# Kernel tuning notes

Measured on AMD Instinct MI355X. Metric: run time of the kernel, lower is better.

## Reference

```python
import jax, jax.numpy as jnp
import numpy as np

B, S, D = 1, 2048, 1024   # batch, seq_len, d_model
E, F, TOP_K = 8, 4096, 2  # num_experts, d_ff, top_k


def setup_inputs() -> dict:
    key = jax.random.key(0)
    k0, k1, k2, k3, k4 = jax.random.split(key, 5)
    s = 0.02
    x = jax.random.normal(k0, (B, S, D), jnp.float32)
    Wr = jax.random.normal(k1, (D, E), jnp.float32) * s          # router
    W1 = jax.random.normal(k2, (E, D, F), jnp.float32) * s       # gate proj per expert
    W3 = jax.random.normal(k3, (E, D, F), jnp.float32) * s       # up proj per expert
    W2 = jax.random.normal(k4, (E, F, D), jnp.float32) * s       # down proj per expert
    return {"x": x, "Wr": Wr, "W1": W1, "W2": W2, "W3": W3}


def reference(x, Wr, W1, W2, W3):
    b, s, d = x.shape
    e = Wr.shape[1]
    xt = x.reshape(b * s, d)                       # [T, D]
    logits = xt @ Wr                               # [T, E]
    top_v, top_i = jax.lax.top_k(logits, TOP_K)    # [T, K]
    probs = jax.nn.softmax(top_v, axis=-1)         # softmax over selected experts
    # combine[t, e] = prob of expert e for token t (0 if not selected)
    combine = jnp.sum(probs[..., None] * jax.nn.one_hot(top_i, e, dtype=xt.dtype), axis=1)  # [T, E]
    # SwiGLU FFN per expert (dense grouped-GEMM form of the gather/scatter loop)
    h = jnp.einsum('td,edf->etf', xt, W1)          # [E, T, F]
    g = jnp.einsum('td,edf->etf', xt, W3)          # [E, T, F]
    y = jnp.einsum('etf,efd->etd', jax.nn.silu(h) * g, W2)  # [E, T, D]
    out = jnp.einsum('etd,te->td', y, combine)     # weighted combine
    return out.reshape(b, s, d)
```

## Files before the change

### kernel.cpp

```cpp
#include <hip/hip_runtime.h>
#include <hip/hip_bf16.h>

#define T_TOK 2048
#define DDIM  1024
#define NEXP  8
#define FDIM  4096
#define ROWS  (4096 + 256)

typedef __attribute__((ext_vector_type(8))) short bf16x8;
typedef __attribute__((ext_vector_type(4))) float f32x4;

#define SBW(n) ((((n) >> 3) ^ (n)) & 7)

__device__ __forceinline__ unsigned short f2b(float f) {
  union { float f; unsigned u; } v; v.f = f;
  unsigned r = v.u + 0x7FFF + ((v.u >> 16) & 1);
  return (unsigned short)(r >> 16);
}
__device__ __forceinline__ float b2f(unsigned short s) {
  union { unsigned u; float f; } v; v.u = ((unsigned)s) << 16;
  return v.f;
}
__device__ __forceinline__ unsigned cvtpk(float lo, float hi) {
  unsigned r;
  asm("v_cvt_pk_bf16_f32 %0, %1, %2" : "=v"(r) : "v"(lo), "v"(hi));
  return r;
}
__device__ __forceinline__ void gl16(const unsigned short* g, unsigned short* l) {
  __builtin_amdgcn_global_load_lds(
      (const __attribute__((address_space(1))) unsigned int*)(const void*)g,
      (__attribute__((address_space(3))) unsigned int*)(void*)l, 16, 0, 0);
}
__device__ __forceinline__ bf16x8 pack8(const float4* br, int c) {
  union { bf16x8 v; unsigned u[4]; } p;
  p.u[0] = cvtpk((&br[0].x)[c], (&br[1].x)[c]);
  p.u[1] = cvtpk((&br[2].x)[c], (&br[3].x)[c]);
  p.u[2] = cvtpk((&br[4].x)[c], (&br[5].x)[c]);
  p.u[3] = cvtpk((&br[6].x)[c], (&br[7].x)[c]);
  return p.v;
}

__global__ void router_kernel(const float* __restrict__ x, const float* __restrict__ Wr,
                              int* __restrict__ cnt, int* __restrict__ tok,
                              float* __restrict__ prb) {
  int t = (blockIdx.x * blockDim.x + threadIdx.x) >> 6;
  int lane = threadIdx.x & 63;
  if (t >= T_TOK) return;
  const float* xr = x + (size_t)t * DDIM;
  float acc[NEXP];
#pragma unroll
  for (int e = 0; e < NEXP; ++e) acc[e] = 0.f;
#pragma unroll
  for (int i = 0; i < 4; ++i) {
    int d0 = lane * 16 + i * 4;
    float4 xv = *reinterpret_cast<const float4*>(xr + d0);
#pragma unroll
    for (int j = 0; j < 4; ++j) {
      float xd = (&xv.x)[j];
      float4 w0 = *reinterpret_cast<const float4*>(Wr + (size_t)(d0 + j) * NEXP);
      float4 w1 = *reinterpret_cast<const float4*>(Wr + (size_t)(d0 + j) * NEXP + 4);
      acc[0] += xd * w0.x; acc[1] += xd * w0.y; acc[2] += xd * w0.z; acc[3] += xd * w0.w;
      acc[4] += xd * w1.x; acc[5] += xd * w1.y; acc[6] += xd * w1.z; acc[7] += xd * w1.w;
    }
  }
#pragma unroll
  for (int off = 32; off >= 1; off >>= 1)
#pragma unroll
    for (int e = 0; e < NEXP; ++e) acc[e] += __shfl_down(acc[e], off);
  if (lane == 0) {
    float v0 = -1e30f, v1 = -1e30f; int i0 = 0, i1 = 0;
#pragma unroll
    for (int e = 0; e < NEXP; ++e) {
      float v = acc[e];
      if (v > v0)      { v1 = v0; i1 = i0; v0 = v; i0 = e; }
      else if (v > v1) { v1 = v; i1 = e; }
    }
    float e1 = __expf(v1 - v0);
    float p0 = 1.f / (1.f + e1);
    float p1 = e1 * p0;
    int s0 = atomicAdd(&cnt[i0], 1);
    tok[i0 * T_TOK + s0] = t; prb[i0 * T_TOK + s0] = p0;
    int s1 = atomicAdd(&cnt[i1], 1);
    tok[i1 * T_TOK + s1] = t; prb[i1 * T_TOK + s1] = p1;
  }
}

__global__ void gather_x_kernel(const float* __restrict__ x, const int* __restrict__ cnt,
                                const int* __restrict__ tok, unsigned short* __restrict__ xg) {
  int gs = blockIdx.x * 4 + (threadIdx.x >> 6);
  int lane = threadIdx.x & 63;
  int s = gs, e = 0;
#pragma unroll
  for (int i = 0; i < NEXP - 1; ++i) {
    int c = cnt[i];
    bool go = (e == i) && (s >= c);
    if (go) { s -= c; e = i + 1; }
  }
  int tk = tok[e * T_TOK + s];
  const float* src = x + (size_t)tk * DDIM;
  unsigned short* dst = xg + (size_t)gs * DDIM;
#pragma unroll
  for (int it = 0; it < 4; ++it) {
    float4 v = *reinterpret_cast<const float4*>(src + it * 256 + lane * 4);
    uint2 p;
    p.x = cvtpk(v.x, v.y);
    p.y = cvtpk(v.z, v.w);
    *reinterpret_cast<uint2*>(dst + it * 256 + lane * 4) = p;
  }
}

__global__ __launch_bounds__(256, 3)
void gemm1ab_kernel(const unsigned short* __restrict__ xg,
                    const float* __restrict__ W1, const float* __restrict__ W3,
                    const int* __restrict__ cnt,
                    unsigned short* __restrict__ act) {
  const int e = blockIdx.z;
  const int cn = cnt[e];
  const int r0 = blockIdx.y * 128;
  if (r0 >= cn) return;
  const int n0 = blockIdx.x * 64;
  int off = 0;
#pragma unroll
  for (int i = 0; i < NEXP; ++i) off += (i < e) ? cnt[i] : 0;

  __shared__ __align__(16) unsigned short sA[128 * 64];
  __shared__ __align__(16) unsigned short sB1[64 * 64];
  __shared__ __align__(16) unsigned short sB3[64 * 64];

  const int tid = threadIdx.x;
  const int lane = tid & 63;
  const int wid = tid >> 6;
  const int wm = wid >> 1, wn = wid & 1;

  const unsigned short* asrc[4];
#pragma unroll
  for (int i = 0; i < 4; ++i) {
    int row = (4 * wid + i) * 8 + (lane >> 3);
    int sl = (lane & 7) ^ (row & 7);
    asrc[i] = xg + (size_t)(off + r0 + row) * DDIM + sl * 8;
  }

  const int lt = tid & 127;
  const int ko = lt >> 4;
  const int nc = (lt & 15) * 4;
  const float* bp = ((tid < 128) ? W1 : W3) + ((size_t)e * DDIM + 8 * ko) * FDIM + n0 + nc;
  unsigned short* wb = (tid < 128) ? sB1 : sB3;
  int woff[4];
#pragma unroll
  for (int c = 0; c < 4; ++c) woff[c] = (nc + c) * 64 + ((ko ^ SBW(nc + c)) * 8);

  float4 br[8];
#define LOADB1(K0)                                                              \
  _Pragma("unroll") for (int r = 0; r < 8; ++r)                                 \
      br[r] = *reinterpret_cast<const float4*>(bp + (size_t)((K0) + r) * FDIM);
#define WRITEB1()                                                               \
  _Pragma("unroll") for (int c = 0; c < 4; ++c)                                 \
      *reinterpret_cast<bf16x8*>(wb + woff[c]) = pack8(br, c);
#define STAGEA1(K0)                                                             \
  _Pragma("unroll") for (int i = 0; i < 4; ++i)                                 \
      gl16(asrc[i] + (K0), &sA[(4 * wid + i) * 512]);

  f32x4 ah[4][2], ag[4][2];
#pragma unroll
  for (int m = 0; m < 4; ++m)
#pragma unroll
    for (int n = 0; n < 2; ++n) { ah[m][n] = (f32x4){0,0,0,0}; ag[m][n] = (f32x4){0,0,0,0}; }

  LOADB1(0);

  for (int k0 = 0; k0 < DDIM; k0 += 64) {
    WRITEB1();
    STAGEA1(k0);
    __syncthreads();
    if (k0 + 64 < DDIM) LOADB1(k0 + 64);
#pragma unroll
    for (int kk = 0; kk < 2; ++kk) {
      int kc8 = kk * 4 + (lane >> 4);
      bf16x8 a[4], b1[2], b3[2];
#pragma unroll
      for (int m = 0; m < 4; ++m) {
        int row = wm * 64 + m * 16 + (lane & 15);
        a[m] = *reinterpret_cast<const bf16x8*>(&sA[row * 64 + ((kc8 ^ (row & 7)) * 8)]);
      }
#pragma unroll
      for (int n = 0; n < 2; ++n) {
        int rowb = wn * 32 + n * 16 + (lane & 15);
        int offb = rowb * 64 + ((kc8 ^ SBW(rowb)) * 8);
        b1[n] = *reinterpret_cast<const bf16x8*>(&sB1[offb]);
        b3[n] = *reinterpret_cast<const bf16x8*>(&sB3[offb]);
      }
#pragma unroll
      for (int m = 0; m < 4; ++m)
#pragma unroll
        for (int n = 0; n < 2; ++n) {
          ah[m][n] = __builtin_amdgcn_mfma_f32_16x16x32_bf16(a[m], b1[n], ah[m][n], 0, 0, 0);
          ag[m][n] = __builtin_amdgcn_mfma_f32_16x16x32_bf16(a[m], b3[n], ag[m][n], 0, 0, 0);
        }
    }
    __syncthreads();
  }
#pragma unroll
  for (int m = 0; m < 4; ++m)
#pragma unroll
    for (int j = 0; j < 4; ++j) {
      int rloc = wm * 64 + m * 16 + (lane >> 4) * 4 + j;
      int s = r0 + rloc;
      if (s < cn) {
        unsigned short* orow = act + (size_t)(off + s) * FDIM + n0 + wn * 32 + (lane & 15);
#pragma unroll
        for (int n = 0; n < 2; ++n) {
          float hv = ah[m][n][j];
          float gv = ag[m][n][j];
          float sg = hv / (1.f + __expf(-hv));
          orow[n * 16] = f2b(sg * gv);
        }
      }
    }
}

__global__ __launch_bounds__(256, 3)
void gemm2d_kernel(const unsigned short* __restrict__ act, const float* __restrict__ W2,
                   const int* __restrict__ cnt, const int* __restrict__ tok,
                   const float* __restrict__ prb, float* __restrict__ out) {
  const int e = blockIdx.z >> 1;
  const int sp = blockIdx.z & 1;
  const int cn = cnt[e];
  const int r0 = blockIdx.y * 128;
  if (r0 >= cn) return;
  const int n0 = blockIdx.x * 128;
  const int kbase = sp * (FDIM / 2);
  int off = 0;
#pragma unroll
  for (int i = 0; i < NEXP; ++i) off += (i < e) ? cnt[i] : 0;

  __shared__ __align__(16) unsigned short sA[128 * 64];
  __shared__ __align__(16) unsigned short sB[128 * 64];

  const int tid = threadIdx.x;
  const int lane = tid & 63;
  const int wid = tid >> 6;
  const int wm = wid >> 1, wn = wid & 1;

  const unsigned short* asrc[4];
#pragma unroll
  for (int i = 0; i < 4; ++i) {
    int row = (4 * wid + i) * 8 + (lane >> 3);
    int sl = (lane & 7) ^ (row & 7);
    asrc[i] = act + (size_t)(off + r0 + row) * FDIM + kbase + sl * 8;
  }

  const int ko = tid >> 5;
  const int nc = (tid & 31) * 4;
  const float* bp = W2 + ((size_t)e * FDIM + kbase + 8 * ko) * DDIM + n0 + nc;
  int woff[4];
#pragma unroll
  for (int c = 0; c < 4; ++c) woff[c] = (nc + c) * 64 + ((ko ^ SBW(nc + c)) * 8);

  float4 br[8];
#define LOADB2(K0)                                                              \
  _Pragma("unroll") for (int r = 0; r < 8; ++r)                                 \
      br[r] = *reinterpret_cast<const float4*>(bp + (size_t)((K0) + r) * DDIM);
#define WRITEB2()                                                               \
  _Pragma("unroll") for (int c = 0; c < 4; ++c)                                 \
      *reinterpret_cast<bf16x8*>(&sB[woff[c]]) = pack8(br, c);
#define STAGEA2(K0)                                                             \
  _Pragma("unroll") for (int i = 0; i < 4; ++i)                                 \
      gl16(asrc[i] + (K0), &sA[(4 * wid + i) * 512]);

  f32x4 acc[4][4];
#pragma unroll
  for (int m = 0; m < 4; ++m)
#pragma unroll
    for (int n = 0; n < 4; ++n) acc[m][n] = (f32x4){0,0,0,0};

  LOADB2(0);

  for (int k0 = 0; k0 < FDIM / 2; k0 += 64) {
    WRITEB2();
    STAGEA2(k0);
    __syncthreads();
    if (k0 + 64 < FDIM / 2) LOADB2(k0 + 64);
#pragma unroll
    for (int kk = 0; kk < 2; ++kk) {
      int kc8 = kk * 4 + (lane >> 4);
      bf16x8 a[4], b[4];
#pragma unroll
      for (int m = 0; m < 4; ++m) {
        int row = wm * 64 + m * 16 + (lane & 15);
        a[m] = *reinterpret_cast<const bf16x8*>(&sA[row * 64 + ((kc8 ^ (row & 7)) * 8)]);
      }
#pragma unroll
      for (int n = 0; n < 4; ++n) {
        int col = wn * 64 + n * 16 + (lane & 15);
        b[n] = *reinterpret_cast<const bf16x8*>(&sB[col * 64 + ((kc8 ^ SBW(col)) * 8)]);
      }
#pragma unroll
      for (int m = 0; m < 4; ++m)
#pragma unroll
        for (int n = 0; n < 4; ++n)
          acc[m][n] = __builtin_amdgcn_mfma_f32_16x16x32_bf16(a[m], b[n], acc[m][n], 0, 0, 0);
    }
    __syncthreads();
  }
#pragma unroll
  for (int m = 0; m < 4; ++m)
#pragma unroll
    for (int j = 0; j < 4; ++j) {
      int rloc = wm * 64 + m * 16 + (lane >> 4) * 4 + j;
      int s = r0 + rloc;
      if (s < cn) {
        int tkn = tok[e * T_TOK + s];
        float p = prb[e * T_TOK + s];
        float* orow = out + (size_t)tkn * DDIM + n0 + wn * 64 + (lane & 15);
#pragma unroll
        for (int n = 0; n < 4; ++n) atomicAdd(&orow[n * 16], p * acc[m][n][j]);
      }
    }
}

extern "C" void kernel_launch(void* const* d_in, const int* in_sizes, int n_in,
                              void* d_out, int out_size, void* d_ws, size_t ws_size,
                              hipStream_t stream) {
  const float* x  = (const float*)d_in[0];
  const float* Wr = (const float*)d_in[1];
  const float* W1 = (const float*)d_in[2];
  const float* W2 = (const float*)d_in[3];
  const float* W3 = (const float*)d_in[4];
  float* out = (float*)d_out;

  char* ws = (char*)d_ws;
  int*   cnt = (int*)ws;
  int*   tok = (int*)(ws + 1024);
  float* prb = (float*)(ws + 1024 + 65536);
  unsigned short* xg  = (unsigned short*)(ws + 256 * 1024);
  unsigned short* act = xg + (size_t)ROWS * DDIM;

  hipMemsetAsync(cnt, 0, NEXP * sizeof(int), stream);
  hipMemsetAsync(d_out, 0, (size_t)out_size * sizeof(float), stream);

  router_kernel<<<T_TOK / 4, 256, 0, stream>>>(x, Wr, cnt, tok, prb);
  gather_x_kernel<<<(2 * T_TOK) / 4, 256, 0, stream>>>(x, cnt, tok, xg);
  gemm1ab_kernel<<<dim3(FDIM / 64, 16, NEXP), 256, 0, stream>>>(xg, W1, W3, cnt, act);
  gemm2d_kernel<<<dim3(DDIM / 128, 16, NEXP * 2), 256, 0, stream>>>(act, W2, cnt, tok, prb, out);
}
```

Baseline: 294.7 us.

## Double-buffer A tile and prefetch B two stages ahead in expert GEMMs

```diff
diff --git a/kernel.cpp b/kernel.cpp
--- a/kernel.cpp
+++ b/kernel.cpp
@@ -39,6 +39,16 @@
   p.u[3] = cvtpk((&br[6].x)[c], (&br[7].x)[c]);
   return p.v;
 }
+
+#define BAR_KEEP12()                                              \
+  __builtin_amdgcn_sched_barrier(0);                              \
+  asm volatile("s_waitcnt vmcnt(12) lgkmcnt(0)" ::: "memory");    \
+  __builtin_amdgcn_s_barrier();                                   \
+  __builtin_amdgcn_sched_barrier(0)
+#define BAR_PLAIN()                                               \
+  __builtin_amdgcn_sched_barrier(0);                              \
+  __builtin_amdgcn_s_barrier();                                   \
+  __builtin_amdgcn_sched_barrier(0)
 
 __global__ void router_kernel(const float* __restrict__ x, const float* __restrict__ Wr,
                               int* __restrict__ cnt, int* __restrict__ tok,
@@ -123,7 +133,7 @@
 #pragma unroll
   for (int i = 0; i < NEXP; ++i) off += (i < e) ? cnt[i] : 0;
 
-  __shared__ __align__(16) unsigned short sA[128 * 64];
+  __shared__ __align__(16) unsigned short sA[2][128 * 64];
   __shared__ __align__(16) unsigned short sB1[64 * 64];
   __shared__ __align__(16) unsigned short sB3[64 * 64];
 
@@ -149,16 +159,16 @@
 #pragma unroll
   for (int c = 0; c < 4; ++c) woff[c] = (nc + c) * 64 + ((ko ^ SBW(nc + c)) * 8);
 
-  float4 br[8];
-#define LOADB1(K0)                                                              \
+  float4 brA[8], brB[8];
+#define LOADB1(BR, K0)                                                          \
   _Pragma("unroll") for (int r = 0; r < 8; ++r)                                 \
-      br[r] = *reinterpret_cast<const float4*>(bp + (size_t)((K0) + r) * FDIM);
-#define WRITEB1()                                                               \
+      BR[r] = *reinterpret_cast<const float4*>(bp + (size_t)((K0) + r) * FDIM);
+#define WRITEB1(BR)                                                             \
   _Pragma("unroll") for (int c = 0; c < 4; ++c)                                 \
-      *reinterpret_cast<bf16x8*>(wb + woff[c]) = pack8(br, c);
-#define STAGEA1(K0)                                                             \
+      *reinterpret_cast<bf16x8*>(wb + woff[c]) = pack8(BR, c);
+#define STAGEA1(K0, BUF)                                                        \
   _Pragma("unroll") for (int i = 0; i < 4; ++i)                                 \
-      gl16(asrc[i] + (K0), &sA[(4 * wid + i) * 512]);
+      gl16(asrc[i] + (K0), &sA[BUF][(4 * wid + i) * 512]);
 
   f32x4 ah[4][2], ag[4][2];
 #pragma unroll
@@ -166,39 +176,51 @@
 #pragma unroll
     for (int n = 0; n < 2; ++n) { ah[m][n] = (f32x4){0,0,0,0}; ag[m][n] = (f32x4){0,0,0,0}; }
 
-  LOADB1(0);
-
-  for (int k0 = 0; k0 < DDIM; k0 += 64) {
-    WRITEB1();
-    STAGEA1(k0);
-    __syncthreads();
-    if (k0 + 64 < DDIM) LOADB1(k0 + 64);
-#pragma unroll
-    for (int kk = 0; kk < 2; ++kk) {
-      int kc8 = kk * 4 + (lane >> 4);
-      bf16x8 a[4], b1[2], b3[2];
-#pragma unroll
-      for (int m = 0; m < 4; ++m) {
-        int row = wm * 64 + m * 16 + (lane & 15);
-        a[m] = *reinterpret_cast<const bf16x8*>(&sA[row * 64 + ((kc8 ^ (row & 7)) * 8)]);
-      }
-#pragma unroll
-      for (int n = 0; n < 2; ++n) {
-        int rowb = wn * 32 + n * 16 + (lane & 15);
-        int offb = rowb * 64 + ((kc8 ^ SBW(rowb)) * 8);
-        b1[n] = *reinterpret_cast<const bf16x8*>(&sB1[offb]);
-        b3[n] = *reinterpret_cast<const bf16x8*>(&sB3[offb]);
-      }
-#pragma unroll
-      for (int m = 0; m < 4; ++m)
-#pragma unroll
-        for (int n = 0; n < 2; ++n) {
-          ah[m][n] = __builtin_amdgcn_mfma_f32_16x16x32_bf16(a[m], b1[n], ah[m][n], 0, 0, 0);
-          ag[m][n] = __builtin_amdgcn_mfma_f32_16x16x32_bf16(a[m], b3[n], ag[m][n], 0, 0, 0);
-        }
-    }
-    __syncthreads();
-  }
+#define MFMA1(CUR)                                                              \
+  _Pragma("unroll") for (int kk = 0; kk < 2; ++kk) {                            \
+    int kc8 = kk * 4 + (lane >> 4);                                             \
+    bf16x8 a[4], b1[2], b3[2];                                                  \
+    _Pragma("unroll") for (int m = 0; m < 4; ++m) {                             \
+      int row = wm * 64 + m * 16 + (lane & 15);                                 \
+      a[m] = *reinterpret_cast<const bf16x8*>(&sA[CUR][row * 64 + ((kc8 ^ (row & 7)) * 8)]); \
+    }                                                                           \
+    _Pragma("unroll") for (int n = 0; n < 2; ++n) {                             \
+      int rowb = wn * 32 + n * 16 + (lane & 15);                                \
+      int offb = rowb * 64 + ((kc8 ^ SBW(rowb)) * 8);                           \
+      b1[n] = *reinterpret_cast<const bf16x8*>(&sB1[offb]);                     \
+      b3[n] = *reinterpret_cast<const bf16x8*>(&sB3[offb]);                     \
+    }                                                                           \
+    _Pragma("unroll") for (int m = 0; m < 4; ++m)                               \
+      _Pragma("unroll") for (int n = 0; n < 2; ++n) {                           \
+        ah[m][n] = __builtin_amdgcn_mfma_f32_16x16x32_bf16(a[m], b1[n], ah[m][n], 0, 0, 0); \
+        ag[m][n] = __builtin_amdgcn_mfma_f32_16x16x32_bf16(a[m], b3[n], ag[m][n], 0, 0, 0); \
+      }                                                                         \
+  }
+
+#define HALF1(K0, BR, CUR)                                                      \
+  WRITEB1(BR);                               \
+  STAGEA1(((K0) + 64) & (DDIM - 1), (CUR) ^ 1);       \
+  LOADB1(BR, ((K0) + 128) & (DDIM - 1));              \
+  BAR_KEEP12();                                                                 \
+  __builtin_amdgcn_s_setprio(1);                                                \
+  MFMA1(CUR);                                                                   \
+  __builtin_amdgcn_s_setprio(0);                                                \
+  BAR_PLAIN();
+
+  LOADB1(brA, 0);
+  LOADB1(brB, 64);
+  STAGEA1(0, 0);
+
+  for (int k0 = 0; k0 < DDIM; k0 += 128) {
+    HALF1(k0, brA, 0);
+    HALF1(k0 + 64, brB, 1);
+  }
+#undef HALF1
+#undef MFMA1
+#undef LOADB1
+#undef WRITEB1
+#undef STAGEA1
+
 #pragma unroll
   for (int m = 0; m < 4; ++m)
 #pragma unroll
@@ -233,7 +255,7 @@
 #pragma unroll
   for (int i = 0; i < NEXP; ++i) off += (i < e) ? cnt[i] : 0;
 
-  __shared__ __align__(16) unsigned short sA[128 * 64];
+  __shared__ __align__(16) unsigned short sA[2][128 * 64];
   __shared__ __align__(16) unsigned short sB[128 * 64];
 
   const int tid = threadIdx.x;
@@ -256,16 +278,16 @@
 #pragma unroll
   for (int c = 0; c < 4; ++c) woff[c] = (nc + c) * 64 + ((ko ^ SBW(nc + c)) * 8);
 
-  float4 br[8];
-#define LOADB2(K0)                                                              \
+  float4 brA[8], brB[8];
+#define LOADB2(BR, K0)                                                          \
   _Pragma("unroll") for (int r = 0; r < 8; ++r)                                 \
-      br[r] = *reinterpret_cast<const float4*>(bp + (size_t)((K0) + r) * DDIM);
-#define WRITEB2()                                                               \
+      BR[r] = *reinterpret_cast<const float4*>(bp + (size_t)((K0) + r) * DDIM);
+#define WRITEB2(BR)                                                             \
   _Pragma("unroll") for (int c = 0; c < 4; ++c)                                 \
-      *reinterpret_cast<bf16x8*>(&sB[woff[c]]) = pack8(br, c);
-#define STAGEA2(K0)                                                             \
+      *reinterpret_cast<bf16x8*>(&sB[woff[c]]) = pack8(BR, c);
+#define STAGEA2(K0, BUF)                                                        \
   _Pragma("unroll") for (int i = 0; i < 4; ++i)                                 \
-      gl16(asrc[i] + (K0), &sA[(4 * wid + i) * 512]);
+      gl16(asrc[i] + (K0), &sA[BUF][(4 * wid + i) * 512]);
 
   f32x4 acc[4][4];
 #pragma unroll
@@ -273,35 +295,47 @@
 #pragma unroll
     for (int n = 0; n < 4; ++n) acc[m][n] = (f32x4){0,0,0,0};
 
-  LOADB2(0);
-
-  for (int k0 = 0; k0 < FDIM / 2; k0 += 64) {
-    WRITEB2();
-    STAGEA2(k0);
-    __syncthreads();
-    if (k0 + 64 < FDIM / 2) LOADB2(k0 + 64);
-#pragma unroll
-    for (int kk = 0; kk < 2; ++kk) {
-      int kc8 = kk * 4 + (lane >> 4);
-      bf16x8 a[4], b[4];
-#pragma unroll
-      for (int m = 0; m < 4; ++m) {
-        int row = wm * 64 + m * 16 + (lane & 15);
-        a[m] = *reinterpret_cast<const bf16x8*>(&sA[row * 64 + ((kc8 ^ (row & 7)) * 8)]);
-      }
-#pragma unroll
-      for (int n = 0; n < 4; ++n) {
-        int col = wn * 64 + n * 16 + (lane & 15);
-        b[n] = *reinterpret_cast<const bf16x8*>(&sB[col * 64 + ((kc8 ^ SBW(col)) * 8)]);
-      }
-#pragma unroll
-      for (int m = 0; m < 4; ++m)
-#pragma unroll
-        for (int n = 0; n < 4; ++n)
-          acc[m][n] = __builtin_amdgcn_mfma_f32_16x16x32_bf16(a[m], b[n], acc[m][n], 0, 0, 0);
-    }
-    __syncthreads();
-  }
+#define MFMA2(CUR)                                                              \
+  _Pragma("unroll") for (int kk = 0; kk < 2; ++kk) {                            \
+    int kc8 = kk * 4 + (lane >> 4);                                             \
+    bf16x8 a[4], b[4];                                                          \
+    _Pragma("unroll") for (int m = 0; m < 4; ++m) {                             \
+      int row = wm * 64 + m * 16 + (lane & 15);                                 \
+      a[m] = *reinterpret_cast<const bf16x8*>(&sA[CUR][row * 64 + ((kc8 ^ (row & 7)) * 8)]); \
+    }                                                                           \
+    _Pragma("unroll") for (int n = 0; n < 4; ++n) {                             \
+      int col = wn * 64 + n * 16 + (lane & 15);                                 \
+      b[n] = *reinterpret_cast<const bf16x8*>(&sB[col * 64 + ((kc8 ^ SBW(col)) * 8)]); \
+    }                                                                           \
+    _Pragma("unroll") for (int m = 0; m < 4; ++m)                               \
+      _Pragma("unroll") for (int n = 0; n < 4; ++n)                             \
+        acc[m][n] = __builtin_amdgcn_mfma_f32_16x16x32_bf16(a[m], b[n], acc[m][n], 0, 0, 0); \
+  }
+
+#define HALF2(K0, BR, CUR)                                                      \
+  WRITEB2(BR);                                                                  \
+  STAGEA2(((K0) + 64) & (FDIM / 2 - 1), (CUR) ^ 1);                             \
+  LOADB2(BR, ((K0) + 128) & (FDIM / 2 - 1));                                    \
+  BAR_KEEP12();                                                                 \
+  __builtin_amdgcn_s_setprio(1);                                                \
+  MFMA2(CUR);                                                                   \
+  __builtin_amdgcn_s_setprio(0);                                                \
+  BAR_PLAIN();
+
+  LOADB2(brA, 0);
+  LOADB2(brB, 64);
+  STAGEA2(0, 0);
+
+  for (int k0 = 0; k0 < FDIM / 2; k0 += 128) {
+    HALF2(k0, brA, 0);
+    HALF2(k0 + 64, brB, 1);
+  }
+#undef HALF2
+#undef MFMA2
+#undef LOADB2
+#undef WRITEB2
+#undef STAGEA2
+
 #pragma unroll
   for (int m = 0; m < 4; ++m)
 #pragma unroll
```

Result: slower. 672.5 us (+128.2%).

## Use 512-thread blocks with 256-row tiles and split warp roles for loading

Applied to the files above, without the earlier changes.

```diff
diff --git a/kernel.cpp b/kernel.cpp
--- a/kernel.cpp
+++ b/kernel.cpp
@@ -109,45 +109,47 @@
   }
 }
 
-__global__ __launch_bounds__(256, 3)
+__global__ __launch_bounds__(512, 2)
 void gemm1ab_kernel(const unsigned short* __restrict__ xg,
                     const float* __restrict__ W1, const float* __restrict__ W3,
                     const int* __restrict__ cnt,
                     unsigned short* __restrict__ act) {
   const int e = blockIdx.z;
   const int cn = cnt[e];
-  const int r0 = blockIdx.y * 128;
+  const int r0 = blockIdx.y * 256;
   if (r0 >= cn) return;
   const int n0 = blockIdx.x * 64;
   int off = 0;
 #pragma unroll
   for (int i = 0; i < NEXP; ++i) off += (i < e) ? cnt[i] : 0;
 
-  __shared__ __align__(16) unsigned short sA[128 * 64];
+  __shared__ __align__(16) unsigned short sA[256 * 64];
   __shared__ __align__(16) unsigned short sB1[64 * 64];
   __shared__ __align__(16) unsigned short sB3[64 * 64];
 
   const int tid = threadIdx.x;
   const int lane = tid & 63;
-  const int wid = tid >> 6;
-  const int wm = wid >> 1, wn = wid & 1;
-
-  const unsigned short* asrc[4];
-#pragma unroll
-  for (int i = 0; i < 4; ++i) {
-    int row = (4 * wid + i) * 8 + (lane >> 3);
-    int sl = (lane & 7) ^ (row & 7);
-    asrc[i] = xg + (size_t)(off + r0 + row) * DDIM + sl * 8;
-  }
+  const int w = tid >> 6;
 
   const int lt = tid & 127;
   const int ko = lt >> 4;
   const int nc = (lt & 15) * 4;
-  const float* bp = ((tid < 128) ? W1 : W3) + ((size_t)e * DDIM + 8 * ko) * FDIM + n0 + nc;
-  unsigned short* wb = (tid < 128) ? sB1 : sB3;
+  const float* bp = ((tid & 128) ? W3 : W1) + ((size_t)e * DDIM + 8 * ko) * FDIM + n0 + nc;
+  unsigned short* wb = (tid & 128) ? sB3 : sB1;
   int woff[4];
 #pragma unroll
   for (int c = 0; c < 4; ++c) woff[c] = (nc + c) * 64 + ((ko ^ SBW(nc + c)) * 8);
+
+  const unsigned short* asrc[8];
+  {
+    int w4 = (tid >> 6) & 3;
+#pragma unroll
+    for (int i = 0; i < 8; ++i) {
+      int row = (w4 * 8 + i) * 8 + (lane >> 3);
+      int sl = (lane & 7) ^ (row & 7);
+      asrc[i] = xg + (size_t)(off + r0 + row) * DDIM + sl * 8;
+    }
+  }
 
   float4 br[8];
 #define LOADB1(K0)                                                              \
@@ -157,58 +159,61 @@
   _Pragma("unroll") for (int c = 0; c < 4; ++c)                                 \
       *reinterpret_cast<bf16x8*>(wb + woff[c]) = pack8(br, c);
 #define STAGEA1(K0)                                                             \
-  _Pragma("unroll") for (int i = 0; i < 4; ++i)                                 \
-      gl16(asrc[i] + (K0), &sA[(4 * wid + i) * 512]);
-
-  f32x4 ah[4][2], ag[4][2];
-#pragma unroll
-  for (int m = 0; m < 4; ++m)
-#pragma unroll
-    for (int n = 0; n < 2; ++n) { ah[m][n] = (f32x4){0,0,0,0}; ag[m][n] = (f32x4){0,0,0,0}; }
-
-  LOADB1(0);
+  {                                                                             \
+    int w4s = (tid >> 6) & 3;                                                   \
+    _Pragma("unroll") for (int i = 0; i < 8; ++i)                               \
+        gl16(asrc[i] + (K0), &sA[(w4s * 8 + i) * 512]);                         \
+  }
+
+  f32x4 ah[2][4], ag[2][4];
+#pragma unroll
+  for (int m = 0; m < 2; ++m)
+#pragma unroll
+    for (int n = 0; n < 4; ++n) { ah[m][n] = (f32x4){0,0,0,0}; ag[m][n] = (f32x4){0,0,0,0}; }
+
+  if (w < 4) LOADB1(0);
 
   for (int k0 = 0; k0 < DDIM; k0 += 64) {
-    WRITEB1();
-    STAGEA1(k0);
+    if (w < 4) { WRITEB1(); } else { STAGEA1(k0); }
     __syncthreads();
-    if (k0 + 64 < DDIM) LOADB1(k0 + 64);
+    if (w < 4 && k0 + 64 < DDIM) LOADB1(k0 + 64);
 #pragma unroll
     for (int kk = 0; kk < 2; ++kk) {
       int kc8 = kk * 4 + (lane >> 4);
-      bf16x8 a[4], b1[2], b3[2];
-#pragma unroll
-      for (int m = 0; m < 4; ++m) {
-        int row = wm * 64 + m * 16 + (lane & 15);
+      bf16x8 a[2], b1[4], b3[4];
+#pragma unroll
+      for (int m = 0; m < 2; ++m) {
+        int row = w * 32 + m * 16 + (lane & 15);
         a[m] = *reinterpret_cast<const bf16x8*>(&sA[row * 64 + ((kc8 ^ (row & 7)) * 8)]);
       }
 #pragma unroll
-      for (int n = 0; n < 2; ++n) {
-        int rowb = wn * 32 + n * 16 + (lane & 15);
+      for (int n = 0; n < 4; ++n) {
+        int rowb = n * 16 + (lane & 15);
         int offb = rowb * 64 + ((kc8 ^ SBW(rowb)) * 8);
         b1[n] = *reinterpret_cast<const bf16x8*>(&sB1[offb]);
         b3[n] = *reinterpret_cast<const bf16x8*>(&sB3[offb]);
       }
 #pragma unroll
-      for (int m = 0; m < 4; ++m)
-#pragma unroll
-        for (int n = 0; n < 2; ++n) {
+      for (int m = 0; m < 2; ++m)
+#pragma unroll
+        for (int n = 0; n < 4; ++n) {
           ah[m][n] = __builtin_amdgcn_mfma_f32_16x16x32_bf16(a[m], b1[n], ah[m][n], 0, 0, 0);
           ag[m][n] = __builtin_amdgcn_mfma_f32_16x16x32_bf16(a[m], b3[n], ag[m][n], 0, 0, 0);
         }
     }
     __syncthreads();
   }
-#pragma unroll
-  for (int m = 0; m < 4; ++m)
+
+#pragma unroll
+  for (int m = 0; m < 2; ++m)
 #pragma unroll
     for (int j = 0; j < 4; ++j) {
-      int rloc = wm * 64 + m * 16 + (lane >> 4) * 4 + j;
+      int rloc = w * 32 + m * 16 + (lane >> 4) * 4 + j;
       int s = r0 + rloc;
       if (s < cn) {
-        unsigned short* orow = act + (size_t)(off + s) * FDIM + n0 + wn * 32 + (lane & 15);
-#pragma unroll
-        for (int n = 0; n < 2; ++n) {
+        unsigned short* orow = act + (size_t)(off + s) * FDIM + n0 + (lane & 15);
+#pragma unroll
+        for (int n = 0; n < 4; ++n) {
           float hv = ah[m][n][j];
           float gv = ag[m][n][j];
           float sg = hv / (1.f + __expf(-hv));
@@ -218,43 +223,46 @@
     }
 }
 
-__global__ __launch_bounds__(256, 3)
+__global__ __launch_bounds__(512, 2)
 void gemm2d_kernel(const unsigned short* __restrict__ act, const float* __restrict__ W2,
                    const int* __restrict__ cnt, const int* __restrict__ tok,
                    const float* __restrict__ prb, float* __restrict__ out) {
-  const int e = blockIdx.z >> 1;
-  const int sp = blockIdx.z & 1;
+  const int e = blockIdx.z >> 2;
+  const int sp = blockIdx.z & 3;
   const int cn = cnt[e];
-  const int r0 = blockIdx.y * 128;
+  const int r0 = blockIdx.y * 256;
   if (r0 >= cn) return;
   const int n0 = blockIdx.x * 128;
-  const int kbase = sp * (FDIM / 2);
+  const int kbase = sp * (FDIM / 4);
   int off = 0;
 #pragma unroll
   for (int i = 0; i < NEXP; ++i) off += (i < e) ? cnt[i] : 0;
 
-  __shared__ __align__(16) unsigned short sA[128 * 64];
+  __shared__ __align__(16) unsigned short sA[256 * 64];
   __shared__ __align__(16) unsigned short sB[128 * 64];
 
   const int tid = threadIdx.x;
   const int lane = tid & 63;
-  const int wid = tid >> 6;
-  const int wm = wid >> 1, wn = wid & 1;
-
-  const unsigned short* asrc[4];
-#pragma unroll
-  for (int i = 0; i < 4; ++i) {
-    int row = (4 * wid + i) * 8 + (lane >> 3);
-    int sl = (lane & 7) ^ (row & 7);
-    asrc[i] = act + (size_t)(off + r0 + row) * FDIM + kbase + sl * 8;
-  }
-
-  const int ko = tid >> 5;
-  const int nc = (tid & 31) * 4;
+  const int w = tid >> 6;
+
+  const int lt = tid & 255;
+  const int ko = lt >> 5;
+  const int nc = (lt & 31) * 4;
   const float* bp = W2 + ((size_t)e * FDIM + kbase + 8 * ko) * DDIM + n0 + nc;
   int woff[4];
 #pragma unroll
   for (int c = 0; c < 4; ++c) woff[c] = (nc + c) * 64 + ((ko ^ SBW(nc + c)) * 8);
+
+  const unsigned short* asrc[8];
+  {
+    int w4 = (tid >> 6) & 3;
+#pragma unroll
+    for (int i = 0; i < 8; ++i) {
+      int row = (w4 * 8 + i) * 8 + (lane >> 3);
+      int sl = (lane & 7) ^ (row & 7);
+      asrc[i] = act + (size_t)(off + r0 + row) * FDIM + kbase + sl * 8;
+    }
+  }
 
   float4 br[8];
 #define LOADB2(K0)                                                              \
@@ -264,56 +272,59 @@
   _Pragma("unroll") for (int c = 0; c < 4; ++c)                                 \
       *reinterpret_cast<bf16x8*>(&sB[woff[c]]) = pack8(br, c);
 #define STAGEA2(K0)                                                             \
-  _Pragma("unroll") for (int i = 0; i < 4; ++i)                                 \
-      gl16(asrc[i] + (K0), &sA[(4 * wid + i) * 512]);
-
-  f32x4 acc[4][4];
-#pragma unroll
-  for (int m = 0; m < 4; ++m)
-#pragma unroll
-    for (int n = 0; n < 4; ++n) acc[m][n] = (f32x4){0,0,0,0};
-
-  LOADB2(0);
-
-  for (int k0 = 0; k0 < FDIM / 2; k0 += 64) {
-    WRITEB2();
-    STAGEA2(k0);
+  {                                                                             \
+    int w4s = (tid >> 6) & 3;                                                   \
+    _Pragma("unroll") for (int i = 0; i < 8; ++i)                               \
+        gl16(asrc[i] + (K0), &sA[(w4s * 8 + i) * 512]);                         \
+  }
+
+  f32x4 acc[2][8];
+#pragma unroll
+  for (int m = 0; m < 2; ++m)
+#pragma unroll
+    for (int n = 0; n < 8; ++n) acc[m][n] = (f32x4){0,0,0,0};
+
+  if (w < 4) LOADB2(0);
+
+  for (int k0 = 0; k0 < FDIM / 4; k0 += 64) {
+    if (w < 4) { WRITEB2(); } else { STAGEA2(k0); }
     __syncthreads();
-    if (k0 + 64 < FDIM / 2) LOADB2(k0 + 64);
+    if (w < 4 && k0 + 64 < FDIM / 4) LOADB2(k0 + 64);
 #pragma unroll
     for (int kk = 0; kk < 2; ++kk) {
       int kc8 = kk * 4 + (lane >> 4);
-      bf16x8 a[4], b[4];
-#pragma unroll
-      for (int m = 0; m < 4; ++m) {
-        int row = wm * 64 + m * 16 + (lane & 15);
+      bf16x8 a[2], b[8];
+#pragma unroll
+      for (int m = 0; m < 2; ++m) {
+        int row = w * 32 + m * 16 + (lane & 15);
         a[m] = *reinterpret_cast<const bf16x8*>(&sA[row * 64 + ((kc8 ^ (row & 7)) * 8)]);
       }
 #pragma unroll
-      for (int n = 0; n < 4; ++n) {
-        int col = wn * 64 + n * 16 + (lane & 15);
+      for (int n = 0; n < 8; ++n) {
+        int col = n * 16 + (lane & 15);
         b[n] = *reinterpret_cast<const bf16x8*>(&sB[col * 64 + ((kc8 ^ SBW(col)) * 8)]);
       }
 #pragma unroll
-      for (int m = 0; m < 4; ++m)
-#pragma unroll
-        for (int n = 0; n < 4; ++n)
+      for (int m = 0; m < 2; ++m)
+#pragma unroll
+        for (int n = 0; n < 8; ++n)
           acc[m][n] = __builtin_amdgcn_mfma_f32_16x16x32_bf16(a[m], b[n], acc[m][n], 0, 0, 0);
     }
     __syncthreads();
   }
-#pragma unroll
-  for (int m = 0; m < 4; ++m)
+
+#pragma unroll
+  for (int m = 0; m < 2; ++m)
 #pragma unroll
     for (int j = 0; j < 4; ++j) {
-      int rloc = wm * 64 + m * 16 + (lane >> 4) * 4 + j;
+      int rloc = w * 32 + m * 16 + (lane >> 4) * 4 + j;
       int s = r0 + rloc;
       if (s < cn) {
         int tkn = tok[e * T_TOK + s];
         float p = prb[e * T_TOK + s];
-        float* orow = out + (size_t)tkn * DDIM + n0 + wn * 64 + (lane & 15);
-#pragma unroll
-        for (int n = 0; n < 4; ++n) atomicAdd(&orow[n * 16], p * acc[m][n][j]);
+        float* orow = out + (size_t)tkn * DDIM + n0 + (lane & 15);
+#pragma unroll
+        for (int n = 0; n < 8; ++n) atomicAdd(&orow[n * 16], p * acc[m][n][j]);
       }
     }
 }
@@ -340,6 +351,6 @@
 
   router_kernel<<<T_TOK / 4, 256, 0, stream>>>(x, Wr, cnt, tok, prb);
   gather_x_kernel<<<(2 * T_TOK) / 4, 256, 0, stream>>>(x, cnt, tok, xg);
-  gemm1ab_kernel<<<dim3(FDIM / 64, 16, NEXP), 256, 0, stream>>>(xg, W1, W3, cnt, act);
-  gemm2d_kernel<<<dim3(DDIM / 128, 16, NEXP * 2), 256, 0, stream>>>(act, W2, cnt, tok, prb, out);
-}
+  gemm1ab_kernel<<<dim3(FDIM / 64, 8, NEXP), 512, 0, stream>>>(xg, W1, W3, cnt, act);
+  gemm2d_kernel<<<dim3(DDIM / 128, 8, NEXP * 4), 512, 0, stream>>>(act, W2, cnt, tok, prb, out);
+}
```

Result: slower. 348.8 us (+18.4%).

## Use 32x32x16 MFMA and 256-row M tiles in both expert GEMMs

Applied to the files above, without the earlier changes.

```diff
diff --git a/kernel.cpp b/kernel.cpp
--- a/kernel.cpp
+++ b/kernel.cpp
@@ -9,6 +9,7 @@
 
 typedef __attribute__((ext_vector_type(8))) short bf16x8;
 typedef __attribute__((ext_vector_type(4))) float f32x4;
+typedef __attribute__((ext_vector_type(16))) float f32x16;
 
 #define SBW(n) ((((n) >> 3) ^ (n)) & 7)
 
@@ -109,33 +110,32 @@
   }
 }
 
-__global__ __launch_bounds__(256, 3)
+__global__ __launch_bounds__(256, 2)
 void gemm1ab_kernel(const unsigned short* __restrict__ xg,
                     const float* __restrict__ W1, const float* __restrict__ W3,
                     const int* __restrict__ cnt,
                     unsigned short* __restrict__ act) {
   const int e = blockIdx.z;
   const int cn = cnt[e];
-  const int r0 = blockIdx.y * 128;
+  const int r0 = blockIdx.y * 256;
   if (r0 >= cn) return;
   const int n0 = blockIdx.x * 64;
   int off = 0;
 #pragma unroll
   for (int i = 0; i < NEXP; ++i) off += (i < e) ? cnt[i] : 0;
 
-  __shared__ __align__(16) unsigned short sA[128 * 64];
+  __shared__ __align__(16) unsigned short sA[256 * 64];
   __shared__ __align__(16) unsigned short sB1[64 * 64];
   __shared__ __align__(16) unsigned short sB3[64 * 64];
 
   const int tid = threadIdx.x;
   const int lane = tid & 63;
   const int wid = tid >> 6;
-  const int wm = wid >> 1, wn = wid & 1;
-
-  const unsigned short* asrc[4];
-#pragma unroll
-  for (int i = 0; i < 4; ++i) {
-    int row = (4 * wid + i) * 8 + (lane >> 3);
+
+  const unsigned short* asrc[8];
+#pragma unroll
+  for (int i = 0; i < 8; ++i) {
+    int row = (wid * 8 + i) * 8 + (lane >> 3);
     int sl = (lane & 7) ^ (row & 7);
     asrc[i] = xg + (size_t)(off + r0 + row) * DDIM + sl * 8;
   }
@@ -157,16 +157,22 @@
   _Pragma("unroll") for (int c = 0; c < 4; ++c)                                 \
       *reinterpret_cast<bf16x8*>(wb + woff[c]) = pack8(br, c);
 #define STAGEA1(K0)                                                             \
-  _Pragma("unroll") for (int i = 0; i < 4; ++i)                                 \
-      gl16(asrc[i] + (K0), &sA[(4 * wid + i) * 512]);
-
-  f32x4 ah[4][2], ag[4][2];
-#pragma unroll
-  for (int m = 0; m < 4; ++m)
-#pragma unroll
-    for (int n = 0; n < 2; ++n) { ah[m][n] = (f32x4){0,0,0,0}; ag[m][n] = (f32x4){0,0,0,0}; }
+  _Pragma("unroll") for (int i = 0; i < 8; ++i)                                 \
+      gl16(asrc[i] + (K0), &sA[(wid * 8 + i) * 512]);
+
+  f32x16 ah[2][2], ag[2][2];
+#pragma unroll
+  for (int m = 0; m < 2; ++m)
+#pragma unroll
+    for (int n = 0; n < 2; ++n) {
+      ah[m][n] = (f32x16)(0.f);
+      ag[m][n] = (f32x16)(0.f);
+    }
 
   LOADB1(0);
+
+  const int l31 = lane & 31;
+  const int khalf = lane >> 5;
 
   for (int k0 = 0; k0 < DDIM; k0 += 64) {
     WRITEB1();
@@ -174,58 +180,59 @@
     __syncthreads();
     if (k0 + 64 < DDIM) LOADB1(k0 + 64);
 #pragma unroll
-    for (int kk = 0; kk < 2; ++kk) {
-      int kc8 = kk * 4 + (lane >> 4);
-      bf16x8 a[4], b1[2], b3[2];
-#pragma unroll
-      for (int m = 0; m < 4; ++m) {
-        int row = wm * 64 + m * 16 + (lane & 15);
-        a[m] = *reinterpret_cast<const bf16x8*>(&sA[row * 64 + ((kc8 ^ (row & 7)) * 8)]);
+    for (int kk = 0; kk < 4; ++kk) {
+      int s = kk * 2 + khalf;
+      bf16x8 a[2], b1[2], b3[2];
+#pragma unroll
+      for (int m = 0; m < 2; ++m) {
+        int row = wid * 64 + m * 32 + l31;
+        a[m] = *reinterpret_cast<const bf16x8*>(&sA[row * 64 + ((s ^ (row & 7)) * 8)]);
       }
 #pragma unroll
       for (int n = 0; n < 2; ++n) {
-        int rowb = wn * 32 + n * 16 + (lane & 15);
-        int offb = rowb * 64 + ((kc8 ^ SBW(rowb)) * 8);
+        int rowb = n * 32 + l31;
+        int offb = rowb * 64 + ((s ^ SBW(rowb)) * 8);
         b1[n] = *reinterpret_cast<const bf16x8*>(&sB1[offb]);
         b3[n] = *reinterpret_cast<const bf16x8*>(&sB3[offb]);
       }
 #pragma unroll
-      for (int m = 0; m < 4; ++m)
+      for (int m = 0; m < 2; ++m)
 #pragma unroll
         for (int n = 0; n < 2; ++n) {
-          ah[m][n] = __builtin_amdgcn_mfma_f32_16x16x32_bf16(a[m], b1[n], ah[m][n], 0, 0, 0);
-          ag[m][n] = __builtin_amdgcn_mfma_f32_16x16x32_bf16(a[m], b3[n], ag[m][n], 0, 0, 0);
+          ah[m][n] = __builtin_amdgcn_mfma_f32_32x32x16_bf16(a[m], b1[n], ah[m][n], 0, 0, 0);
+          ag[m][n] = __builtin_amdgcn_mfma_f32_32x32x16_bf16(a[m], b3[n], ag[m][n], 0, 0, 0);
         }
     }
     __syncthreads();
   }
-#pragma unroll
-  for (int m = 0; m < 4; ++m)
-#pragma unroll
-    for (int j = 0; j < 4; ++j) {
-      int rloc = wm * 64 + m * 16 + (lane >> 4) * 4 + j;
+
+#pragma unroll
+  for (int m = 0; m < 2; ++m)
+#pragma unroll
+    for (int r = 0; r < 16; ++r) {
+      int rloc = wid * 64 + m * 32 + (r & 3) + 8 * (r >> 2) + 4 * khalf;
       int s = r0 + rloc;
       if (s < cn) {
-        unsigned short* orow = act + (size_t)(off + s) * FDIM + n0 + wn * 32 + (lane & 15);
+        unsigned short* orow = act + (size_t)(off + s) * FDIM + n0 + l31;
 #pragma unroll
         for (int n = 0; n < 2; ++n) {
-          float hv = ah[m][n][j];
-          float gv = ag[m][n][j];
+          float hv = ah[m][n][r];
+          float gv = ag[m][n][r];
           float sg = hv / (1.f + __expf(-hv));
-          orow[n * 16] = f2b(sg * gv);
+          orow[n * 32] = f2b(sg * gv);
         }
       }
     }
 }
 
-__global__ __launch_bounds__(256, 3)
+__global__ __launch_bounds__(256, 2)
 void gemm2d_kernel(const unsigned short* __restrict__ act, const float* __restrict__ W2,
                    const int* __restrict__ cnt, const int* __restrict__ tok,
                    const float* __restrict__ prb, float* __restrict__ out) {
   const int e = blockIdx.z >> 1;
   const int sp = blockIdx.z & 1;
   const int cn = cnt[e];
-  const int r0 = blockIdx.y * 128;
+  const int r0 = blockIdx.y * 256;
   if (r0 >= cn) return;
   const int n0 = blockIdx.x * 128;
   const int kbase = sp * (FDIM / 2);
@@ -233,18 +240,17 @@
 #pragma unroll
   for (int i = 0; i < NEXP; ++i) off += (i < e) ? cnt[i] : 0;
 
-  __shared__ __align__(16) unsigned short sA[128 * 64];
+  __shared__ __align__(16) unsigned short sA[256 * 64];
   __shared__ __align__(16) unsigned short sB[128 * 64];
 
   const int tid = threadIdx.x;
   const int lane = tid & 63;
   const int wid = tid >> 6;
-  const int wm = wid >> 1, wn = wid & 1;
-
-  const unsigned short* asrc[4];
-#pragma unroll
-  for (int i = 0; i < 4; ++i) {
-    int row = (4 * wid + i) * 8 + (lane >> 3);
+
+  const unsigned short* asrc[8];
+#pragma unroll
+  for (int i = 0; i < 8; ++i) {
+    int row = (wid * 8 + i) * 8 + (lane >> 3);
     int sl = (lane & 7) ^ (row & 7);
     asrc[i] = act + (size_t)(off + r0 + row) * FDIM + kbase + sl * 8;
   }
@@ -264,16 +270,19 @@
   _Pragma("unroll") for (int c = 0; c < 4; ++c)                                 \
       *reinterpret_cast<bf16x8*>(&sB[woff[c]]) = pack8(br, c);
 #define STAGEA2(K0)                                                             \
-  _Pragma("unroll") for (int i = 0; i < 4; ++i)                                 \
-      gl16(asrc[i] + (K0), &sA[(4 * wid + i) * 512]);
-
-  f32x4 acc[4][4];
-#pragma unroll
-  for (int m = 0; m < 4; ++m)
-#pragma unroll
-    for (int n = 0; n < 4; ++n) acc[m][n] = (f32x4){0,0,0,0};
+  _Pragma("unroll") for (int i = 0; i < 8; ++i)                                 \
+      gl16(asrc[i] + (K0), &sA[(wid * 8 + i) * 512]);
+
+  f32x16 acc[2][4];
+#pragma unroll
+  for (int m = 0; m < 2; ++m)
+#pragma unroll
+    for (int n = 0; n < 4; ++n) acc[m][n] = (f32x16)(0.f);
 
   LOADB2(0);
+
+  const int l31 = lane & 31;
+  const int khalf = lane >> 5;
 
   for (int k0 = 0; k0 < FDIM / 2; k0 += 64) {
     WRITEB2();
@@ -281,39 +290,40 @@
     __syncthreads();
     if (k0 + 64 < FDIM / 2) LOADB2(k0 + 64);
 #pragma unroll
-    for (int kk = 0; kk < 2; ++kk) {
-      int kc8 = kk * 4 + (lane >> 4);
-      bf16x8 a[4], b[4];
-#pragma unroll
-      for (int m = 0; m < 4; ++m) {
-        int row = wm * 64 + m * 16 + (lane & 15);
-        a[m] = *reinterpret_cast<const bf16x8*>(&sA[row * 64 + ((kc8 ^ (row & 7)) * 8)]);
+    for (int kk = 0; kk < 4; ++kk) {
+      int s = kk * 2 + khalf;
+      bf16x8 a[2], b[4];
+#pragma unroll
+      for (int m = 0; m < 2; ++m) {
+        int row = wid * 64 + m * 32 + l31;
+        a[m] = *reinterpret_cast<const bf16x8*>(&sA[row * 64 + ((s ^ (row & 7)) * 8)]);
       }
 #pragma unroll
       for (int n = 0; n < 4; ++n) {
-        int col = wn * 64 + n * 16 + (lane & 15);
-        b[n] = *reinterpret_cast<const bf16x8*>(&sB[col * 64 + ((kc8 ^ SBW(col)) * 8)]);
-      }
-#pragma unroll
-      for (int m = 0; m < 4; ++m)
+        int col = n * 32 + l31;
+        b[n] = *reinterpret_cast<const bf16x8*>(&sB[col * 64 + ((s ^ SBW(col)) * 8)]);
+      }
+#pragma unroll
+      for (int m = 0; m < 2; ++m)
 #pragma unroll
         for (int n = 0; n < 4; ++n)
-          acc[m][n] = __builtin_amdgcn_mfma_f32_16x16x32_bf16(a[m], b[n], acc[m][n], 0, 0, 0);
+          acc[m][n] = __builtin_amdgcn_mfma_f32_32x32x16_bf16(a[m], b[n], acc[m][n], 0, 0, 0);
     }
     __syncthreads();
   }
-#pragma unroll
-  for (int m = 0; m < 4; ++m)
-#pragma unroll
-    for (int j = 0; j < 4; ++j) {
-      int rloc = wm * 64 + m * 16 + (lane >> 4) * 4 + j;
+
+#pragma unroll
+  for (int m = 0; m < 2; ++m)
+#pragma unroll
+    for (int r = 0; r < 16; ++r) {
+      int rloc = wid * 64 + m * 32 + (r & 3) + 8 * (r >> 2) + 4 * khalf;
       int s = r0 + rloc;
       if (s < cn) {
         int tkn = tok[e * T_TOK + s];
         float p = prb[e * T_TOK + s];
-        float* orow = out + (size_t)tkn * DDIM + n0 + wn * 64 + (lane & 15);
-#pragma unroll
-        for (int n = 0; n < 4; ++n) atomicAdd(&orow[n * 16], p * acc[m][n][j]);
+        float* orow = out + (size_t)tkn * DDIM + n0 + l31;
+#pragma unroll
+        for (int n = 0; n < 4; ++n) atomicAdd(&orow[n * 32], p * acc[m][n][r]);
       }
     }
 }
@@ -340,6 +350,6 @@
 
   router_kernel<<<T_TOK / 4, 256, 0, stream>>>(x, Wr, cnt, tok, prb);
   gather_x_kernel<<<(2 * T_TOK) / 4, 256, 0, stream>>>(x, cnt, tok, xg);
-  gemm1ab_kernel<<<dim3(FDIM / 64, 16, NEXP), 256, 0, stream>>>(xg, W1, W3, cnt, act);
-  gemm2d_kernel<<<dim3(DDIM / 128, 16, NEXP * 2), 256, 0, stream>>>(act, W2, cnt, tok, prb, out);
-}
+  gemm1ab_kernel<<<dim3(FDIM / 64, 8, NEXP), 256, 0, stream>>>(xg, W1, W3, cnt, act);
+  gemm2d_kernel<<<dim3(DDIM / 128, 8, NEXP * 2), 256, 0, stream>>>(act, W2, cnt, tok, prb, out);
+}
```

Result: slower. 302.9 us (+2.8%).
